# Performance work log

Measured on AMD Instinct MI355X. Metric: run time of the kernel, lower is better.

Reference implementation:

```python
import jax, jax.numpy as jnp
import numpy as np

BS, L, D, N = 4, 2048, 1024, 16

def setup_inputs() -> dict:
    key = jax.random.key(0)
    ks = jax.random.split(key, 8)
    s = 1.0 / np.sqrt(D)
    x  = jax.random.normal(ks[0], (BS, L, D), dtype=jnp.float32)
    # torch Linear params; stored transposed so y = x @ W + b
    W1 = jax.random.uniform(ks[1], (D, D), jnp.float32, -s, s)
    b1 = jax.random.uniform(ks[2], (D,),   jnp.float32, -s, s)
    W2 = jax.random.uniform(ks[3], (D, N), jnp.float32, -s, s)
    b2 = jax.random.uniform(ks[4], (N,),   jnp.float32, -s, s)
    W3 = jax.random.uniform(ks[5], (D, N), jnp.float32, -s, s)
    b3 = jax.random.uniform(ks[6], (N,),   jnp.float32, -s, s)
    A  = jax.random.normal(ks[7], (D, N),  jnp.float32) * np.sqrt(2.0 / (D + N))  # xavier
    return {"x": x, "W1": W1, "b1": b1, "W2": W2, "b2": b2, "W3": W3, "b3": b3, "A": A}

def reference(x, W1, b1, W2, b2, W3, b3, A):
    # S6 forward (non-recurrent branch).
    B = x @ W2 + b2                     # (b,l,n)
    C = x @ W3 + b3                     # (b,l,n)
    delta = jax.nn.softplus(x @ W1 + b1)  # (b,l,d)
    # dA = exp(einsum('bld,dn->bldn', delta, A)) is multiplied by an all-zero h
    # in the original forward, so it does not affect the output (dead code under DCE).
    dB = jnp.einsum('bld,bln->bldn', delta, B)   # (b,l,d,n) -- 512 MB intermediate
    h = x[..., None] * dB                         # (b,l,d,n)
    y = jnp.einsum('bln,bldn->bld', C, h)         # (b,l,d)
    return y
```

## Files before the change

kernel.cpp:

```cpp
#include <hip/hip_runtime.h>
#include <hip/hip_bf16.h>
#include <math.h>


namespace {

constexpr int Dd   = 1024;
constexpr int ROWS = 8192;

typedef __bf16 bf16x8 __attribute__((ext_vector_type(8)));
typedef float  floatx4 __attribute__((ext_vector_type(4)));

__device__ __forceinline__ float softplus_fast(float v) {
    float l = __logf(1.0f + __expf(v));
    return v > 15.0f ? v : l;
}
__device__ __forceinline__ float bf_lo(unsigned short u) {
    union { unsigned q; float f; } c; c.q = ((unsigned)u) << 16; return c.f;
}

__device__ __forceinline__ void gld_lds16(const __bf16* g, __bf16* l) {
    __builtin_amdgcn_global_load_lds(
        (const __attribute__((address_space(1))) void*)g,
        (__attribute__((address_space(3))) void*)l, 16, 0, 0);
}

#define BAR()    asm volatile("s_barrier" ::: "memory")
#define LGKM0()  asm volatile("s_waitcnt lgkmcnt(0)" ::: "memory")
#define VMCNT(n) asm volatile("s_waitcnt vmcnt(" #n ")" ::: "memory")

__global__ __launch_bounds__(256) void w23_kernel(
    const float* __restrict__ W2, const float* __restrict__ W3,
    __bf16* __restrict__ W2t, __bf16* __restrict__ W3t)
{
    const int t  = threadIdx.x;
    const int n  = t >> 4;
    const int k0 = blockIdx.x * 64 + (t & 15) * 4;
    ushort4 a, b;
    union { __bf16 h; unsigned short u; } c;
    c.h = (__bf16)W2[(size_t)(k0 + 0) * 16 + n]; a.x = c.u;
    c.h = (__bf16)W2[(size_t)(k0 + 1) * 16 + n]; a.y = c.u;
    c.h = (__bf16)W2[(size_t)(k0 + 2) * 16 + n]; a.z = c.u;
    c.h = (__bf16)W2[(size_t)(k0 + 3) * 16 + n]; a.w = c.u;
    c.h = (__bf16)W3[(size_t)(k0 + 0) * 16 + n]; b.x = c.u;
    c.h = (__bf16)W3[(size_t)(k0 + 1) * 16 + n]; b.y = c.u;
    c.h = (__bf16)W3[(size_t)(k0 + 2) * 16 + n]; b.z = c.u;
    c.h = (__bf16)W3[(size_t)(k0 + 3) * 16 + n]; b.w = c.u;
    *(ushort4*)&W2t[(size_t)n * Dd + k0] = a;
    *(ushort4*)&W3t[(size_t)n * Dd + k0] = b;
}

__global__ __launch_bounds__(256, 4) void prep_kernel(
    const float* __restrict__ X, const float* __restrict__ W1,
    const __bf16* __restrict__ W2t, const float* __restrict__ b2,
    const __bf16* __restrict__ W3t, const float* __restrict__ b3,
    __bf16* __restrict__ Xb, __bf16* __restrict__ W1t, float* __restrict__ Sv)
{
    const int t = threadIdx.x;

    if (blockIdx.x >= 512) {
        __shared__ __bf16 tile[64][66];
        const int bidx = blockIdx.x - 512;
        const int bi = bidx >> 4, bj = bidx & 15;
        const int c = t & 63, r4 = t >> 6;
        #pragma unroll
        for (int i = 0; i < 16; ++i) {
            const int r = i * 4 + r4;
            tile[r][c] = (__bf16)W1[(size_t)(bi * 64 + r) * Dd + bj * 64 + c];
        }
        __syncthreads();
        #pragma unroll
        for (int i = 0; i < 16; ++i) {
            const int r = i * 4 + r4;
            W1t[(size_t)(bj * 64 + r) * Dd + bi * 64 + c] = tile[c][r];
        }
        return;
    }

    __shared__ float red[4][2][16][16];
    const int w = t >> 6, lane = t & 63;
    const int l15 = lane & 15, quad = lane >> 4;
    const int row0 = blockIdx.x * 16;
    const int kw = w * 256;
    const size_t xoff = (size_t)(row0 + l15) * Dd;
    const size_t woff = (size_t)l15 * Dd;

    floatx4 acc0 = {0.f, 0.f, 0.f, 0.f}, acc1 = {0.f, 0.f, 0.f, 0.f};
    #pragma unroll
    for (int ks = 0; ks < 8; ++ks) {
        const int k0 = kw + ks * 32 + quad * 8;
        const float4 xa = *(const float4*)&X[xoff + k0];
        const float4 xb = *(const float4*)&X[xoff + k0 + 4];
        bf16x8 af;
        af[0] = (__bf16)xa.x; af[1] = (__bf16)xa.y;
        af[2] = (__bf16)xa.z; af[3] = (__bf16)xa.w;
        af[4] = (__bf16)xb.x; af[5] = (__bf16)xb.y;
        af[6] = (__bf16)xb.z; af[7] = (__bf16)xb.w;
        *(bf16x8*)&Xb[xoff + k0] = af;
        const bf16x8 w2f = *(const bf16x8*)&W2t[woff + k0];
        const bf16x8 w3f = *(const bf16x8*)&W3t[woff + k0];
        acc0 = __builtin_amdgcn_mfma_f32_16x16x32_bf16(af, w2f, acc0, 0, 0, 0);
        acc1 = __builtin_amdgcn_mfma_f32_16x16x32_bf16(af, w3f, acc1, 0, 0, 0);
    }
    #pragma unroll
    for (int r = 0; r < 4; ++r) {
        red[w][0][quad * 4 + r][l15] = acc0[r];
        red[w][1][quad * 4 + r][l15] = acc1[r];
    }
    __syncthreads();
    {
        const int r = t >> 4, n = t & 15;
        float B = b2[n], C = b3[n];
        #pragma unroll
        for (int ww = 0; ww < 4; ++ww) {
            B += red[ww][0][r][n];
            C += red[ww][1][r][n];
        }
        float p = B * C;
        p += __shfl_xor(p, 1); p += __shfl_xor(p, 2);
        p += __shfl_xor(p, 4); p += __shfl_xor(p, 8);
        if (n == 0) Sv[row0 + r] = p;
    }
}

#define MF(mt, nt, a_, b_) \
    acc[mt][nt] = __builtin_amdgcn_mfma_f32_16x16x32_bf16(a_, b_, acc[mt][nt], 0, 0, 0)
#define MFMA16() do { \
    __builtin_amdgcn_s_setprio(1); \
    MF(0, 0, af0, bf0); MF(0, 1, af0, bf1); MF(0, 2, af0, bf2); MF(0, 3, af0, bf3); \
    MF(1, 0, af1, bf0); MF(1, 1, af1, bf1); MF(1, 2, af1, bf2); MF(1, 3, af1, bf3); \
    MF(2, 0, af2, bf0); MF(2, 1, af2, bf1); MF(2, 2, af2, bf2); MF(2, 3, af2, bf3); \
    MF(3, 0, af3, bf0); MF(3, 1, af3, bf1); MF(3, 2, af3, bf2); MF(3, 3, af3, bf3); \
    __builtin_amdgcn_s_setprio(0); } while (0)

#define TILE(B0_, B1_, NX1_, KA_, KB_, S1_, S2_, N1_, N2_) do { \
    bf16x8 af0, af1, af2, af3, bf0, bf1, bf2, bf3; \
     \
    af0 = rdA(B0_, 0); af1 = rdA(B0_, 1); af2 = rdA(B0_, 2); af3 = rdA(B0_, 3); \
    bf0 = rdB(B0_, 0); bf1 = rdB(B0_, 1); bf2 = rdB(B0_, 2); bf3 = rdB(B0_, 3); \
    if (S1_) { stageA(NX1_, KA_); stageB(NX1_, KA_); } \
    BAR(); LGKM0(); MFMA16(); VMCNT(N1_); BAR(); \
     \
    af0 = rdA(B1_, 0); af1 = rdA(B1_, 1); af2 = rdA(B1_, 2); af3 = rdA(B1_, 3); \
    bf0 = rdB(B1_, 0); bf1 = rdB(B1_, 1); bf2 = rdB(B1_, 2); bf3 = rdB(B1_, 3); \
    if (S2_) { stageA(B0_, KB_); stageB(B0_, KB_); } \
    BAR(); LGKM0(); MFMA16(); VMCNT(N2_); BAR(); \
} while (0)

__global__ __launch_bounds__(512, 2) void gemm_kernel(
    const __bf16* __restrict__ Xb, const __bf16* __restrict__ W1t,
    const float* __restrict__ Sv, const float* __restrict__ b1,
    float* __restrict__ Y)
{
    __shared__ __attribute__((aligned(16))) __bf16 lds[73728];
    const int t = threadIdx.x, lane = t & 63;
    const int w = t >> 6, wm = w & 3, wn = w >> 2;
    const int l15 = lane & 15, quad = lane >> 4;
    const int xcd = blockIdx.x & 7, loc = blockIdx.x >> 3;
    const int rb = xcd + 8 * (loc & 3);
    const int cb = loc >> 2;
    const int row0 = rb * 256, col0 = cb * 128;

    floatx4 acc[4][4] = {};

    const __bf16* gAs[2]; int dAs[2];
    #pragma unroll
    for (int i = 0; i < 2; ++i) {
        const int d = i * 512 + t, r = d >> 2, cp = d & 3, c = cp ^ ((r >> 1) & 3);
        gAs[i] = Xb + (size_t)(row0 + r) * Dd + c * 8;
        dAs[i] = d * 8;
    }
    const __bf16* gBs; int dBs;
    {
        const int d = t, r = d >> 2, cp = d & 3, c = cp ^ ((r >> 1) & 3);
        gBs = W1t + (size_t)(col0 + r) * Dd + c * 8;
        dBs = d * 8;
    }

    auto stageA = [&](int slot, int kb) {
        #pragma unroll
        for (int i = 0; i < 2; ++i)
            gld_lds16(gAs[i] + kb, &lds[slot * 8192 + dAs[i]]);
    };
    auto stageB = [&](int slot, int kb) {
        gld_lds16(gBs + kb, &lds[49152 + slot * 4096 + dBs]);
    };

    const int sc  = (quad ^ ((l15 >> 1) & 3)) * 8;
    const int aro = (wm * 64 + l15) * 32 + sc;
    const int bro = (wn * 64 + l15) * 32 + sc;

    auto rdA = [&](int slot, int mt) {
        return *(const bf16x8*)&lds[slot * 8192 + aro + mt * 512];
    };
    auto rdB = [&](int slot, int nt) {
        return *(const bf16x8*)&lds[49152 + slot * 4096 + bro + nt * 512];
    };

    stageA(0, 0);   stageB(0, 0);
    stageA(1, 32);  stageB(1, 32);
    stageA(2, 64);  stageB(2, 64);
    stageA(3, 96);  stageB(3, 96);
    stageA(4, 128); stageB(4, 128);
    VMCNT(12); BAR();

    #pragma unroll 1
    for (int uu = 0; uu < 4; ++uu) {
        const int ku = uu * 192;
        TILE(0, 1, 5, ku + 160, ku + 192, true, true, 12, 12);
        TILE(2, 3, 1, ku + 224, ku + 256, true, true, 12, 12);
        TILE(4, 5, 3, ku + 288, ku + 320, true, true, 12, 12);
    }
    TILE(0, 1, 5, 928, 960, true,  true,  12, 12);
    TILE(2, 3, 1, 992, 0,   true,  false, 12, 9);
    TILE(4, 5, 3, 0,   0,   false, false, 6,  3);
    TILE(0, 1, 5, 0,   0,   false, false, 0,  0);

    float bias[4];
    #pragma unroll
    for (int nt = 0; nt < 4; ++nt) bias[nt] = b1[col0 + wn * 64 + nt * 16 + l15];

    #pragma unroll
    for (int mt = 0; mt < 4; ++mt) {
        #pragma unroll
        for (int rr = 0; rr < 4; ++rr) {
            const int row = row0 + wm * 64 + mt * 16 + quad * 4 + rr;
            const float sv = Sv[row];
            const unsigned short* xrow =
                (const unsigned short*)(Xb + (size_t)row * Dd + col0);
            float* yrow = Y + (size_t)row * Dd + col0;
            #pragma unroll
            for (int nt = 0; nt < 4; ++nt) {
                const int cl = wn * 64 + nt * 16 + l15;
                const float v  = acc[mt][nt][rr] + bias[nt];
                const float sp = softplus_fast(v);
                yrow[cl] = bf_lo(xrow[cl]) * sp * sv;
            }
        }
    }
}

}

extern "C" void kernel_launch(void* const* d_in, const int* in_sizes, int n_in,
                              void* d_out, int out_size, void* d_ws, size_t ws_size,
                              hipStream_t stream)
{
    const float* X  = (const float*)d_in[0];
    const float* W1 = (const float*)d_in[1];
    const float* b1 = (const float*)d_in[2];
    const float* W2 = (const float*)d_in[3];
    const float* b2 = (const float*)d_in[4];
    const float* W3 = (const float*)d_in[5];
    const float* b3 = (const float*)d_in[6];
    float* Y = (float*)d_out;

    char* ws = (char*)d_ws;
    __bf16* Xb  = (__bf16*)ws;
    __bf16* W1t = (__bf16*)(ws + 16777216);
    float*  Sv  = (float*) (ws + 16777216 + 2097152);
    __bf16* W2t = (__bf16*)(ws + 16777216 + 2097152 + 32768);
    __bf16* W3t = (__bf16*)(ws + 16777216 + 2097152 + 65536);

    hipLaunchKernelGGL(w23_kernel, dim3(16), dim3(256), 0, stream, W2, W3, W2t, W3t);
    hipLaunchKernelGGL(prep_kernel, dim3(768), dim3(256), 0, stream,
                       X, W1, W2t, b2, W3t, b3, Xb, W1t, Sv);
    hipLaunchKernelGGL(gemm_kernel, dim3((ROWS / 256) * (Dd / 128)), dim3(512), 0, stream,
                       Xb, W1t, Sv, b1, Y);
}
```

Measured before the change: 128.5 us.

## Fuse prep and GEMM kernels into one cooperative kernel with grid sync

Merges the W2/W3 conversion, the W1 transpose, the X-to-bf16 cast with the B·C row-sum, and the main GEMM into a single cooperative launch of 256 blocks, separated by a grid-wide barrier. Each block now converts the full W2/W3 into LDS itself instead of reading a pre-transposed global copy, which removes the separate w23 kernel. The aim is to eliminate two kernel launches and their inter-kernel gaps. In exchange it adds redundant per-block W2/W3 loading, a grid.sync cost, and requires all 256 blocks to be co-resident.

New measurement: 174.8 us. 36.0% more time.

```diff
diff --git a/kernel.cpp b/kernel.cpp
--- a/kernel.cpp
+++ b/kernel.cpp
@@ -1,7 +1,10 @@
 #include <hip/hip_runtime.h>
+#include <hip/hip_cooperative_groups.h>
 #include <hip/hip_bf16.h>
 #include <math.h>
 
+
+namespace cg = cooperative_groups;
 
 namespace {
 
@@ -28,100 +31,6 @@
 #define BAR()    asm volatile("s_barrier" ::: "memory")
 #define LGKM0()  asm volatile("s_waitcnt lgkmcnt(0)" ::: "memory")
 #define VMCNT(n) asm volatile("s_waitcnt vmcnt(" #n ")" ::: "memory")
-
-__global__ __launch_bounds__(256) void w23_kernel(
-    const float* __restrict__ W2, const float* __restrict__ W3,
-    __bf16* __restrict__ W2t, __bf16* __restrict__ W3t)
-{
-    const int t  = threadIdx.x;
-    const int n  = t >> 4;
-    const int k0 = blockIdx.x * 64 + (t & 15) * 4;
-    ushort4 a, b;
-    union { __bf16 h; unsigned short u; } c;
-    c.h = (__bf16)W2[(size_t)(k0 + 0) * 16 + n]; a.x = c.u;
-    c.h = (__bf16)W2[(size_t)(k0 + 1) * 16 + n]; a.y = c.u;
-    c.h = (__bf16)W2[(size_t)(k0 + 2) * 16 + n]; a.z = c.u;
-    c.h = (__bf16)W2[(size_t)(k0 + 3) * 16 + n]; a.w = c.u;
-    c.h = (__bf16)W3[(size_t)(k0 + 0) * 16 + n]; b.x = c.u;
-    c.h = (__bf16)W3[(size_t)(k0 + 1) * 16 + n]; b.y = c.u;
-    c.h = (__bf16)W3[(size_t)(k0 + 2) * 16 + n]; b.z = c.u;
-    c.h = (__bf16)W3[(size_t)(k0 + 3) * 16 + n]; b.w = c.u;
-    *(ushort4*)&W2t[(size_t)n * Dd + k0] = a;
-    *(ushort4*)&W3t[(size_t)n * Dd + k0] = b;
-}
-
-__global__ __launch_bounds__(256, 4) void prep_kernel(
-    const float* __restrict__ X, const float* __restrict__ W1,
-    const __bf16* __restrict__ W2t, const float* __restrict__ b2,
-    const __bf16* __restrict__ W3t, const float* __restrict__ b3,
-    __bf16* __restrict__ Xb, __bf16* __restrict__ W1t, float* __restrict__ Sv)
-{
-    const int t = threadIdx.x;
-
-    if (blockIdx.x >= 512) {
-        __shared__ __bf16 tile[64][66];
-        const int bidx = blockIdx.x - 512;
-        const int bi = bidx >> 4, bj = bidx & 15;
-        const int c = t & 63, r4 = t >> 6;
-        #pragma unroll
-        for (int i = 0; i < 16; ++i) {
-            const int r = i * 4 + r4;
-            tile[r][c] = (__bf16)W1[(size_t)(bi * 64 + r) * Dd + bj * 64 + c];
-        }
-        __syncthreads();
-        #pragma unroll
-        for (int i = 0; i < 16; ++i) {
-            const int r = i * 4 + r4;
-            W1t[(size_t)(bj * 64 + r) * Dd + bi * 64 + c] = tile[c][r];
-        }
-        return;
-    }
-
-    __shared__ float red[4][2][16][16];
-    const int w = t >> 6, lane = t & 63;
-    const int l15 = lane & 15, quad = lane >> 4;
-    const int row0 = blockIdx.x * 16;
-    const int kw = w * 256;
-    const size_t xoff = (size_t)(row0 + l15) * Dd;
-    const size_t woff = (size_t)l15 * Dd;
-
-    floatx4 acc0 = {0.f, 0.f, 0.f, 0.f}, acc1 = {0.f, 0.f, 0.f, 0.f};
-    #pragma unroll
-    for (int ks = 0; ks < 8; ++ks) {
-        const int k0 = kw + ks * 32 + quad * 8;
-        const float4 xa = *(const float4*)&X[xoff + k0];
-        const float4 xb = *(const float4*)&X[xoff + k0 + 4];
-        bf16x8 af;
-        af[0] = (__bf16)xa.x; af[1] = (__bf16)xa.y;
-        af[2] = (__bf16)xa.z; af[3] = (__bf16)xa.w;
-        af[4] = (__bf16)xb.x; af[5] = (__bf16)xb.y;
-        af[6] = (__bf16)xb.z; af[7] = (__bf16)xb.w;
-        *(bf16x8*)&Xb[xoff + k0] = af;
-        const bf16x8 w2f = *(const bf16x8*)&W2t[woff + k0];
-        const bf16x8 w3f = *(const bf16x8*)&W3t[woff + k0];
-        acc0 = __builtin_amdgcn_mfma_f32_16x16x32_bf16(af, w2f, acc0, 0, 0, 0);
-        acc1 = __builtin_amdgcn_mfma_f32_16x16x32_bf16(af, w3f, acc1, 0, 0, 0);
-    }
-    #pragma unroll
-    for (int r = 0; r < 4; ++r) {
-        red[w][0][quad * 4 + r][l15] = acc0[r];
-        red[w][1][quad * 4 + r][l15] = acc1[r];
-    }
-    __syncthreads();
-    {
-        const int r = t >> 4, n = t & 15;
-        float B = b2[n], C = b3[n];
-        #pragma unroll
-        for (int ww = 0; ww < 4; ++ww) {
-            B += red[ww][0][r][n];
-            C += red[ww][1][r][n];
-        }
-        float p = B * C;
-        p += __shfl_xor(p, 1); p += __shfl_xor(p, 2);
-        p += __shfl_xor(p, 4); p += __shfl_xor(p, 8);
-        if (n == 0) Sv[row0 + r] = p;
-    }
-}
 
 #define MF(mt, nt, a_, b_) \
     acc[mt][nt] = __builtin_amdgcn_mfma_f32_16x16x32_bf16(a_, b_, acc[mt][nt], 0, 0, 0)
@@ -147,94 +56,182 @@
     BAR(); LGKM0(); MFMA16(); VMCNT(N2_); BAR(); \
 } while (0)
 
-__global__ __launch_bounds__(512, 2) void gemm_kernel(
-    const __bf16* __restrict__ Xb, const __bf16* __restrict__ W1t,
-    const float* __restrict__ Sv, const float* __restrict__ b1,
+__global__ __launch_bounds__(512, 2) void fused_kernel(
+    const float* __restrict__ X,  const float* __restrict__ W1,
+    const float* __restrict__ b1, const float* __restrict__ W2,
+    const float* __restrict__ b2, const float* __restrict__ W3,
+    const float* __restrict__ b3, __bf16* __restrict__ Xb,
+    __bf16* __restrict__ W1t, float* __restrict__ Sv,
     float* __restrict__ Y)
 {
     __shared__ __attribute__((aligned(16))) __bf16 lds[73728];
     const int t = threadIdx.x, lane = t & 63;
-    const int w = t >> 6, wm = w & 3, wn = w >> 2;
     const int l15 = lane & 15, quad = lane >> 4;
-    const int xcd = blockIdx.x & 7, loc = blockIdx.x >> 3;
-    const int rb = xcd + 8 * (loc & 3);
-    const int cb = loc >> 2;
-    const int row0 = rb * 256, col0 = cb * 128;
-
-    floatx4 acc[4][4] = {};
-
-    const __bf16* gAs[2]; int dAs[2];
-    #pragma unroll
-    for (int i = 0; i < 2; ++i) {
-        const int d = i * 512 + t, r = d >> 2, cp = d & 3, c = cp ^ ((r >> 1) & 3);
-        gAs[i] = Xb + (size_t)(row0 + r) * Dd + c * 8;
-        dAs[i] = d * 8;
+    const int blk = blockIdx.x;
+
+    {
+        __bf16* W2L = lds;
+        __bf16* W3L = lds + 16512;
+        float*  redL = (float*)((char*)lds + 66048);
+        __bf16 (*tileL)[66] = (__bf16(*)[66])((char*)lds + 82432);
+
+        const float4* W2v = (const float4*)W2;
+        const float4* W3v = (const float4*)W3;
+        #pragma unroll
+        for (int jj = 0; jj < 8; ++jj) {
+            const int q = t + jj * 512;
+            const int k = q >> 2, n0 = (q & 3) << 2;
+            const float4 v2 = W2v[q];
+            const float4 v3 = W3v[q];
+            W2L[(n0 + 0) * 1032 + k] = (__bf16)v2.x;
+            W2L[(n0 + 1) * 1032 + k] = (__bf16)v2.y;
+            W2L[(n0 + 2) * 1032 + k] = (__bf16)v2.z;
+            W2L[(n0 + 3) * 1032 + k] = (__bf16)v2.w;
+            W3L[(n0 + 0) * 1032 + k] = (__bf16)v3.x;
+            W3L[(n0 + 1) * 1032 + k] = (__bf16)v3.y;
+            W3L[(n0 + 2) * 1032 + k] = (__bf16)v3.z;
+            W3L[(n0 + 3) * 1032 + k] = (__bf16)v3.w;
+        }
+        const int bi = blk >> 4, bj = blk & 15;
+        const int tc = t & 63, r8 = t >> 6;
+        #pragma unroll
+        for (int i = 0; i < 8; ++i) {
+            const int r = i * 8 + r8;
+            tileL[r][tc] = (__bf16)W1[(size_t)(bi * 64 + r) * Dd + bj * 64 + tc];
+        }
+        __syncthreads();
+        #pragma unroll
+        for (int i = 0; i < 8; ++i) {
+            const int r = i * 8 + r8;
+            W1t[(size_t)(bj * 64 + r) * Dd + bi * 64 + tc] = tileL[tc][r];
+        }
+
+        const int w = t >> 6, g = w >> 2, kw = (w & 3) * 256;
+        const int row0p = blk * 32;
+        const size_t xoff = (size_t)(row0p + g * 16 + l15) * Dd;
+
+        floatx4 acc0 = {0.f, 0.f, 0.f, 0.f}, acc1 = {0.f, 0.f, 0.f, 0.f};
+        #pragma unroll
+        for (int ks = 0; ks < 8; ++ks) {
+            const int k0 = kw + ks * 32 + quad * 8;
+            const float4 xa = *(const float4*)&X[xoff + k0];
+            const float4 xc = *(const float4*)&X[xoff + k0 + 4];
+            bf16x8 af;
+            af[0] = (__bf16)xa.x; af[1] = (__bf16)xa.y;
+            af[2] = (__bf16)xa.z; af[3] = (__bf16)xa.w;
+            af[4] = (__bf16)xc.x; af[5] = (__bf16)xc.y;
+            af[6] = (__bf16)xc.z; af[7] = (__bf16)xc.w;
+            *(bf16x8*)&Xb[xoff + k0] = af;
+            const bf16x8 w2f = *(const bf16x8*)&W2L[l15 * 1032 + k0];
+            const bf16x8 w3f = *(const bf16x8*)&W3L[l15 * 1032 + k0];
+            acc0 = __builtin_amdgcn_mfma_f32_16x16x32_bf16(af, w2f, acc0, 0, 0, 0);
+            acc1 = __builtin_amdgcn_mfma_f32_16x16x32_bf16(af, w3f, acc1, 0, 0, 0);
+        }
+        #pragma unroll
+        for (int r = 0; r < 4; ++r) {
+            redL[w * 512 + (quad * 4 + r) * 16 + l15]       = acc0[r];
+            redL[w * 512 + 256 + (quad * 4 + r) * 16 + l15] = acc1[r];
+        }
+        __syncthreads();
+        {
+            const int g2 = t >> 8, tt = t & 255, r = tt >> 4, n = tt & 15;
+            float Bv = b2[n], Cv = b3[n];
+            #pragma unroll
+            for (int ww = 0; ww < 4; ++ww) {
+                Bv += redL[(g2 * 4 + ww) * 512 + r * 16 + n];
+                Cv += redL[(g2 * 4 + ww) * 512 + 256 + r * 16 + n];
+            }
+            float pp = Bv * Cv;
+            pp += __shfl_xor(pp, 1); pp += __shfl_xor(pp, 2);
+            pp += __shfl_xor(pp, 4); pp += __shfl_xor(pp, 8);
+            if (n == 0) Sv[row0p + g2 * 16 + r] = pp;
+        }
     }
-    const __bf16* gBs; int dBs;
+
+    cg::this_grid().sync();
+
     {
-        const int d = t, r = d >> 2, cp = d & 3, c = cp ^ ((r >> 1) & 3);
-        gBs = W1t + (size_t)(col0 + r) * Dd + c * 8;
-        dBs = d * 8;
-    }
-
-    auto stageA = [&](int slot, int kb) {
-        #pragma unroll
-        for (int i = 0; i < 2; ++i)
-            gld_lds16(gAs[i] + kb, &lds[slot * 8192 + dAs[i]]);
-    };
-    auto stageB = [&](int slot, int kb) {
-        gld_lds16(gBs + kb, &lds[49152 + slot * 4096 + dBs]);
-    };
-
-    const int sc  = (quad ^ ((l15 >> 1) & 3)) * 8;
-    const int aro = (wm * 64 + l15) * 32 + sc;
-    const int bro = (wn * 64 + l15) * 32 + sc;
-
-    auto rdA = [&](int slot, int mt) {
-        return *(const bf16x8*)&lds[slot * 8192 + aro + mt * 512];
-    };
-    auto rdB = [&](int slot, int nt) {
-        return *(const bf16x8*)&lds[49152 + slot * 4096 + bro + nt * 512];
-    };
-
-    stageA(0, 0);   stageB(0, 0);
-    stageA(1, 32);  stageB(1, 32);
-    stageA(2, 64);  stageB(2, 64);
-    stageA(3, 96);  stageB(3, 96);
-    stageA(4, 128); stageB(4, 128);
-    VMCNT(12); BAR();
-
-    #pragma unroll 1
-    for (int uu = 0; uu < 4; ++uu) {
-        const int ku = uu * 192;
-        TILE(0, 1, 5, ku + 160, ku + 192, true, true, 12, 12);
-        TILE(2, 3, 1, ku + 224, ku + 256, true, true, 12, 12);
-        TILE(4, 5, 3, ku + 288, ku + 320, true, true, 12, 12);
-    }
-    TILE(0, 1, 5, 928, 960, true,  true,  12, 12);
-    TILE(2, 3, 1, 992, 0,   true,  false, 12, 9);
-    TILE(4, 5, 3, 0,   0,   false, false, 6,  3);
-    TILE(0, 1, 5, 0,   0,   false, false, 0,  0);
-
-    float bias[4];
-    #pragma unroll
-    for (int nt = 0; nt < 4; ++nt) bias[nt] = b1[col0 + wn * 64 + nt * 16 + l15];
-
-    #pragma unroll
-    for (int mt = 0; mt < 4; ++mt) {
-        #pragma unroll
-        for (int rr = 0; rr < 4; ++rr) {
-            const int row = row0 + wm * 64 + mt * 16 + quad * 4 + rr;
-            const float sv = Sv[row];
-            const unsigned short* xrow =
-                (const unsigned short*)(Xb + (size_t)row * Dd + col0);
-            float* yrow = Y + (size_t)row * Dd + col0;
+        const int w = t >> 6, wm = w & 3, wn = w >> 2;
+        const int xcd = blk & 7, loc = blk >> 3;
+        const int rb = xcd + 8 * (loc & 3);
+        const int cb = loc >> 2;
+        const int row0 = rb * 256, col0 = cb * 128;
+
+        floatx4 acc[4][4] = {};
+
+        const __bf16* gAs[2]; int dAs[2];
+        #pragma unroll
+        for (int i = 0; i < 2; ++i) {
+            const int d = i * 512 + t, r = d >> 2, cp = d & 3, c = cp ^ ((r >> 1) & 3);
+            gAs[i] = Xb + (size_t)(row0 + r) * Dd + c * 8;
+            dAs[i] = d * 8;
+        }
+        const __bf16* gBs; int dBs;
+        {
+            const int d = t, r = d >> 2, cp = d & 3, c = cp ^ ((r >> 1) & 3);
+            gBs = W1t + (size_t)(col0 + r) * Dd + c * 8;
+            dBs = d * 8;
+        }
+
+        auto stageA = [&](int slot, int kb) {
             #pragma unroll
-            for (int nt = 0; nt < 4; ++nt) {
-                const int cl = wn * 64 + nt * 16 + l15;
-                const float v  = acc[mt][nt][rr] + bias[nt];
-                const float sp = softplus_fast(v);
-                yrow[cl] = bf_lo(xrow[cl]) * sp * sv;
+            for (int i = 0; i < 2; ++i)
+                gld_lds16(gAs[i] + kb, &lds[slot * 8192 + dAs[i]]);
+        };
+        auto stageB = [&](int slot, int kb) {
+            gld_lds16(gBs + kb, &lds[49152 + slot * 4096 + dBs]);
+        };
+
+        const int sc  = (quad ^ ((l15 >> 1) & 3)) * 8;
+        const int aro = (wm * 64 + l15) * 32 + sc;
+        const int bro = (wn * 64 + l15) * 32 + sc;
+
+        auto rdA = [&](int slot, int mt) {
+            return *(const bf16x8*)&lds[slot * 8192 + aro + mt * 512];
+        };
+        auto rdB = [&](int slot, int nt) {
+            return *(const bf16x8*)&lds[49152 + slot * 4096 + bro + nt * 512];
+        };
+
+        stageA(0, 0);   stageB(0, 0);
+        stageA(1, 32);  stageB(1, 32);
+        stageA(2, 64);  stageB(2, 64);
+        stageA(3, 96);  stageB(3, 96);
+        stageA(4, 128); stageB(4, 128);
+        VMCNT(12); BAR();
+
+        #pragma unroll 1
+        for (int uu = 0; uu < 4; ++uu) {
+            const int ku = uu * 192;
+            TILE(0, 1, 5, ku + 160, ku + 192, true, true, 12, 12);
+            TILE(2, 3, 1, ku + 224, ku + 256, true, true, 12, 12);
+            TILE(4, 5, 3, ku + 288, ku + 320, true, true, 12, 12);
+        }
+        TILE(0, 1, 5, 928, 960, true,  true,  12, 12);
+        TILE(2, 3, 1, 992, 0,   true,  false, 12, 9);
+        TILE(4, 5, 3, 0,   0,   false, false, 6,  3);
+        TILE(0, 1, 5, 0,   0,   false, false, 0,  0);
+
+        float bias[4];
+        #pragma unroll
+        for (int nt = 0; nt < 4; ++nt) bias[nt] = b1[col0 + wn * 64 + nt * 16 + l15];
+
+        #pragma unroll
+        for (int mt = 0; mt < 4; ++mt) {
+            #pragma unroll
+            for (int rr = 0; rr < 4; ++rr) {
+                const int row = row0 + wm * 64 + mt * 16 + quad * 4 + rr;
+                const float sv = Sv[row];
+                const unsigned short* xrow =
+                    (const unsigned short*)(Xb + (size_t)row * Dd + col0);
+                float* yrow = Y + (size_t)row * Dd + col0;
+                #pragma unroll
+                for (int nt = 0; nt < 4; ++nt) {
+                    const int cl = wn * 64 + nt * 16 + l15;
+                    const float v  = acc[mt][nt][rr] + bias[nt];
+                    const float sp = softplus_fast(v);
+                    yrow[cl] = bf_lo(xrow[cl]) * sp * sv;
+                }
             }
         }
     }
@@ -259,12 +256,11 @@
     __bf16* Xb  = (__bf16*)ws;
     __bf16* W1t = (__bf16*)(ws + 16777216);
     float*  Sv  = (float*) (ws + 16777216 + 2097152);
-    __bf16* W2t = (__bf16*)(ws + 16777216 + 2097152 + 32768);
-    __bf16* W3t = (__bf16*)(ws + 16777216 + 2097152 + 65536);
-
-    hipLaunchKernelGGL(w23_kernel, dim3(16), dim3(256), 0, stream, W2, W3, W2t, W3t);
-    hipLaunchKernelGGL(prep_kernel, dim3(768), dim3(256), 0, stream,
-                       X, W1, W2t, b2, W3t, b3, Xb, W1t, Sv);
-    hipLaunchKernelGGL(gemm_kernel, dim3((ROWS / 256) * (Dd / 128)), dim3(512), 0, stream,
-                       Xb, W1t, Sv, b1, Y);
-}
+
+    void* args[] = {
+        (void*)&X, (void*)&W1, (void*)&b1, (void*)&W2, (void*)&b2,
+        (void*)&W3, (void*)&b3, (void*)&Xb, (void*)&W1t, (void*)&Sv, (void*)&Y
+    };
+    hipLaunchCooperativeKernel(reinterpret_cast<void*>(fused_kernel),
+                               dim3(256), dim3(512), args, 0, stream);
+}
```
